# Performance work log

Measured on AMD Instinct MI355X. Metric: run time of the kernel, lower is better.

The kernel has to match this reference:

```python
import jax, jax.numpy as jnp
import numpy as np

WIN_LEN = 400
HOP = 100
NFFT = 512


def _make_kernel():
    # rfft of identity -> DFT basis, truncated to window length
    fb = np.fft.rfft(np.eye(NFFT))[:WIN_LEN]          # [WIN_LEN, NFFT//2+1] complex
    kernel = np.concatenate([fb.real, fb.imag], axis=1).T  # [2*(NFFT//2+1), WIN_LEN]
    # periodic (fftbins=True) Hamming window, as scipy.signal.get_window('hamming', N, fftbins=True)
    n = np.arange(WIN_LEN)
    window = (0.54 - 0.46 * np.cos(2.0 * np.pi * n / WIN_LEN)).astype(np.float32)
    kernel = kernel.astype(np.float32)[:, None, :] * window  # [514, 1, WIN_LEN]
    return jnp.asarray(kernel)


def setup_inputs() -> dict:
    key = jax.random.key(0)
    x = jax.random.normal(key, (32, 480000), dtype=jnp.float32)  # [B, T] raw audio
    return {"x": x, "weight": _make_kernel()}


def reference(x, weight):
    # x: [B, T] -> [B, 1, T]; pad both sides by (window_len - hop)
    pad = WIN_LEN - HOP
    xp = jnp.pad(x[:, None, :], ((0, 0), (0, 0), (pad, pad)))
    # strided conv against fixed Fourier basis -> [B, 2*(NFFT//2+1), n_frames]
    out = jax.lax.conv_general_dilated(
        xp, weight,
        window_strides=(HOP,),
        padding='VALID',
        dimension_numbers=('NCH', 'OIH', 'NCH'),
    )
    return out
```

## Files before the change

kernel.cpp:

```cpp
#include <hip/hip_runtime.h>
#include <hip/hip_bf16.h>


#define T_LEN   480000
#define NF      4803
#define C_OUT   514
#define HOP     100
#define WIN     400
#define BM      128
#define BN      64
#define WSTR    424
#define XPS     487040
#define XP_TOTAL (32 * XPS)
#define WP_ROWS 576
#define WP_ELEMS (WP_ROWS * WSTR)
#define WP_BYTE_OFF ((size_t)XP_TOTAL * 2)
#define WS_NEEDED (WP_BYTE_OFF + (size_t)WP_ELEMS * 2)
#define MT_CNT  38
#define NT_CNT  9
#define NTILES  (NT_CNT * MT_CNT * 32)
#define TPNT    (MT_CNT * 32)
#define XSEG    13312
#define NBLK    512

typedef __attribute__((ext_vector_type(8))) short short8;
typedef __attribute__((ext_vector_type(4))) float f32x4;

__device__ __forceinline__ unsigned short f2bf(float f) {
    unsigned int u = __float_as_uint(f);
    u += 0x7FFFu + ((u >> 16) & 1u);
    return (unsigned short)(u >> 16);
}

__device__ __forceinline__ void gl_lds16(const unsigned short* g, unsigned short* l) {
    __builtin_amdgcn_global_load_lds(
        (const __attribute__((address_space(1))) unsigned int*)(g),
        (__attribute__((address_space(3))) unsigned int*)(l), 16, 0, 0);
}

__global__ void cvt_x_kernel(const float* __restrict__ x, unsigned short* __restrict__ xp) {
    const int t = blockIdx.x * 256 + threadIdx.x;
    const int b  = t / (XPS / 4);
    const int i4 = t - b * (XPS / 4);
    const int i  = i4 * 4;
    const int g  = i - 300;
    ushort4 h;
    if (g >= 0 && g + 3 < T_LEN) {
        const float4 f = *(const float4*)(x + (size_t)b * T_LEN + g);
        h.x = f2bf(f.x); h.y = f2bf(f.y); h.z = f2bf(f.z); h.w = f2bf(f.w);
    } else {
        const float* xb = x + (size_t)b * T_LEN;
        h.x = (g + 0 >= 0 && g + 0 < T_LEN) ? f2bf(xb[g + 0]) : 0;
        h.y = (g + 1 >= 0 && g + 1 < T_LEN) ? f2bf(xb[g + 1]) : 0;
        h.z = (g + 2 >= 0 && g + 2 < T_LEN) ? f2bf(xb[g + 2]) : 0;
        h.w = (g + 3 >= 0 && g + 3 < T_LEN) ? f2bf(xb[g + 3]) : 0;
    }
    *(ushort4*)(xp + (size_t)b * XPS + i) = h;
}

__global__ void cvt_w_kernel(const float* __restrict__ w, unsigned short* __restrict__ wp) {
    const int t = blockIdx.x * 256 + threadIdx.x;
    if (t >= WP_ELEMS) return;
    const int c = t / WSTR;
    const int k = t - c * WSTR;
    wp[t] = (c < C_OUT && k < WIN) ? f2bf(w[(size_t)c * WIN + k]) : 0;
}

__device__ __forceinline__ void decode_tile(int t, int& nt, int& b, int& mt) {
    nt = t / TPNT;
    const int rem = t - nt * TPNT;
    b  = rem / MT_CNT;
    mt = rem - b * MT_CNT;
}

__global__ __launch_bounds__(512, 4)
void stft_gemm(const unsigned short* __restrict__ xp,
               const unsigned short* __restrict__ wp,
               float* __restrict__ out) {
    __shared__ unsigned short w_s[BN * WSTR];
    __shared__ unsigned short x_s[XSEG];

    const int tid  = threadIdx.x;
    const int lane = tid & 63;
    const int wv   = tid >> 6;

    const int id  = blockIdx.x;
    const int t0  = id * 21 + ((id < 192) ? id : 192);
    const int nti = 21 + (id < 192 ? 1 : 0);

    int nt, b, mt;
    decode_tile(t0, nt, b, mt);

    {
        const unsigned short* wg = wp + (size_t)nt * (BN * WSTR);
        #pragma unroll
        for (int c = wv; c < 53; c += 8) {
            const int idx = (c << 6) + lane;
            gl_lds16(wg + idx * 8, w_s + idx * 8);
        }
        const unsigned short* xg = xp + (size_t)b * XPS + mt * (BM * HOP);
        #pragma unroll
        for (int c = wv; c < 26; c += 8) {
            const int idx = (c << 6) + lane;
            gl_lds16(xg + idx * 8, x_s + idx * 8);
        }
    }
    __syncthreads();

    const int q4 = lane >> 4;
    const int lm = lane & 15;
    const int wr = wv & 3;
    const int wc = wv >> 2;

    int aoff[2];
    #pragma unroll
    for (int mi = 0; mi < 2; ++mi) aoff[mi] = (wr * 32 + mi * 16 + lm) * HOP + q4 * 8;
    int boff[2];
    #pragma unroll
    for (int ni = 0; ni < 2; ++ni) boff[ni] = (wc * 32 + ni * 16 + lm) * WSTR + q4 * 8;

    for (int ti = 0; ti < nti; ++ti) {
        f32x4 acc[2][2];
        #pragma unroll
        for (int mi = 0; mi < 2; ++mi)
            #pragma unroll
            for (int ni = 0; ni < 2; ++ni)
                acc[mi][ni] = (f32x4){0.f, 0.f, 0.f, 0.f};

        #pragma unroll
        for (int kc = 0; kc < 13; ++kc) {
            const int k = kc * 32;
            union { short8 v; unsigned long long u[2]; } au[2];
            #pragma unroll
            for (int mi = 0; mi < 2; ++mi) {
                const unsigned long long* p = (const unsigned long long*)(x_s + aoff[mi] + k);
                au[mi].u[0] = p[0]; au[mi].u[1] = p[1];
            }
            #pragma unroll
            for (int ni = 0; ni < 2; ++ni) {
                const short8 bf = *(const short8*)(&w_s[boff[ni] + k]);
                #pragma unroll
                for (int mi = 0; mi < 2; ++mi)
                    acc[mi][ni] = __builtin_amdgcn_mfma_f32_16x16x32_bf16(au[mi].v, bf, acc[mi][ni], 0, 0, 0);
            }
        }

        __syncthreads();

        int nnt = nt, nb = 0, nmt = 0;
        const bool have_next = (ti + 1 < nti);
        if (have_next) {
            decode_tile(t0 + ti + 1, nnt, nb, nmt);
            const unsigned short* xg = xp + (size_t)nb * XPS + nmt * (BM * HOP);
            #pragma unroll
            for (int c = wv; c < 26; c += 8) {
                const int idx = (c << 6) + lane;
                gl_lds16(xg + idx * 8, x_s + idx * 8);
            }
            if (nnt != nt) {
                const unsigned short* wg = wp + (size_t)nnt * (BN * WSTR);
                #pragma unroll
                for (int c = wv; c < 53; c += 8) {
                    const int idx = (c << 6) + lane;
                    gl_lds16(wg + idx * 8, w_s + idx * 8);
                }
            }
        }

        float* ob = out + (size_t)b * C_OUT * NF;
        const int f_base = mt * BM + wr * 32 + q4 * 4;
        const int c_base = nt * BN + wc * 32 + lm;
        #pragma unroll
        for (int mi = 0; mi < 2; ++mi) {
            const int fg = f_base + mi * 16;
            const bool fok = (fg + 3 < NF);
            #pragma unroll
            for (int ni = 0; ni < 2; ++ni) {
                const int cg = c_base + ni * 16;
                if (cg < C_OUT) {
                    float* op = ob + (size_t)cg * NF + fg;
                    if (fok) {
                        op[0] = acc[mi][ni][0]; op[1] = acc[mi][ni][1];
                        op[2] = acc[mi][ni][2]; op[3] = acc[mi][ni][3];
                    } else {
                        #pragma unroll
                        for (int rI = 0; rI < 4; ++rI)
                            if (fg + rI < NF) op[rI] = acc[mi][ni][rI];
                    }
                }
            }
        }

        __syncthreads();
        nt = nnt; b = nb; mt = nmt;
    }
}

#define SEG 13120
__global__ __launch_bounds__(256, 2)
void conv_stft_fallback(const float* __restrict__ x,
                        const float* __restrict__ w,
                        float* __restrict__ out) {
    __shared__ short x_s[SEG];
    __shared__ short w_s[BN * WSTR];
    const int tid = threadIdx.x;
    const int nt  = blockIdx.x;
    const int mt  = blockIdx.y;
    const int b   = blockIdx.z;
    const int s0 = mt * (BM * HOP) - 300;
    const float* xb = x + (size_t)b * T_LEN;
    for (int v = tid; v < SEG / 4; v += 256) {
        int g = s0 + v * 4;
        float f0, f1, f2, f3;
        if (g >= 0 && g + 3 < T_LEN) {
            const float4 f = *(const float4*)(xb + g);
            f0 = f.x; f1 = f.y; f2 = f.z; f3 = f.w;
        } else {
            f0 = (g + 0 >= 0 && g + 0 < T_LEN) ? xb[g + 0] : 0.f;
            f1 = (g + 1 >= 0 && g + 1 < T_LEN) ? xb[g + 1] : 0.f;
            f2 = (g + 2 >= 0 && g + 2 < T_LEN) ? xb[g + 2] : 0.f;
            f3 = (g + 3 >= 0 && g + 3 < T_LEN) ? xb[g + 3] : 0.f;
        }
        ushort4 h; h.x = f2bf(f0); h.y = f2bf(f1); h.z = f2bf(f2); h.w = f2bf(f3);
        *(ushort4*)(&x_s[v * 4]) = h;
    }
    for (int s = tid; s < BN * 106; s += 256) {
        const int r  = s / 106;
        const int gk = s - r * 106;
        const int c  = nt * BN + r;
        ushort4 h = make_ushort4(0, 0, 0, 0);
        if (gk < 100 && c < C_OUT) {
            const float4 f = *(const float4*)(w + (size_t)c * WIN + gk * 4);
            h.x = f2bf(f.x); h.y = f2bf(f.y); h.z = f2bf(f.z); h.w = f2bf(f.w);
        }
        if (gk * 4 < WSTR) *(ushort4*)(&w_s[r * WSTR + gk * 4]) = h;
    }
    __syncthreads();
    const int lane = tid & 63, wv = tid >> 6, q = lane >> 4, lm = lane & 15;
    f32x4 acc[2][4];
    #pragma unroll
    for (int mi = 0; mi < 2; ++mi)
        #pragma unroll
        for (int ni = 0; ni < 4; ++ni) acc[mi][ni] = (f32x4){0.f,0.f,0.f,0.f};
    const int a0 = (wv * 32 + lm) * HOP + q * 8;
    const int a1 = a0 + 16 * HOP;
    int boff[4];
    #pragma unroll
    for (int ni = 0; ni < 4; ++ni) boff[ni] = (ni * 16 + lm) * WSTR + q * 8;
    #pragma unroll
    for (int kc = 0; kc < 13; ++kc) {
        const int k = kc * 32;
        union { short8 v; unsigned long long u[2]; } au0, au1;
        const unsigned long long* p0 = (const unsigned long long*)(x_s + a0 + k);
        const unsigned long long* p1 = (const unsigned long long*)(x_s + a1 + k);
        au0.u[0] = p0[0]; au0.u[1] = p0[1];
        au1.u[0] = p1[0]; au1.u[1] = p1[1];
        #pragma unroll
        for (int ni = 0; ni < 4; ++ni) {
            const short8 bf = *(const short8*)(&w_s[boff[ni] + k]);
            acc[0][ni] = __builtin_amdgcn_mfma_f32_16x16x32_bf16(au0.v, bf, acc[0][ni], 0, 0, 0);
            acc[1][ni] = __builtin_amdgcn_mfma_f32_16x16x32_bf16(au1.v, bf, acc[1][ni], 0, 0, 0);
        }
    }
    float* ob = out + (size_t)b * C_OUT * NF;
    const int f_base = mt * BM + wv * 32 + q * 4;
    const int c_base = nt * BN + lm;
    #pragma unroll
    for (int mi = 0; mi < 2; ++mi) {
        #pragma unroll
        for (int ni = 0; ni < 4; ++ni) {
            const int cg = c_base + ni * 16;
            if (cg < C_OUT) {
                float* op = ob + (size_t)cg * NF;
                #pragma unroll
                for (int r = 0; r < 4; ++r) {
                    const int fg = f_base + mi * 16 + r;
                    if (fg < NF) op[fg] = acc[mi][ni][r];
                }
            }
        }
    }
}

extern "C" void kernel_launch(void* const* d_in, const int* in_sizes, int n_in,
                              void* d_out, int out_size, void* d_ws, size_t ws_size,
                              hipStream_t stream) {
    const float* x = (const float*)d_in[0];
    const float* w = (const float*)d_in[1];
    float* out = (float*)d_out;

    if (ws_size >= WS_NEEDED) {
        unsigned short* xp = (unsigned short*)d_ws;
        unsigned short* wp = (unsigned short*)((char*)d_ws + WP_BYTE_OFF);
        cvt_x_kernel<<<XP_TOTAL / 4 / 256, 256, 0, stream>>>(x, xp);
        cvt_w_kernel<<<(WP_ELEMS + 255) / 256, 256, 0, stream>>>(w, wp);
        stft_gemm<<<dim3(NBLK), 512, 0, stream>>>(xp, wp, out);
    } else {
        dim3 grid(NT_CNT, MT_CNT, 32);
        conv_stft_fallback<<<grid, 256, 0, stream>>>(x, w, out);
    }
}
```

Before: 460.2 us.

## Stream pre-swizzled B fragments from global and loop all N-tiles per x segment

Weights are converted into an MFMA-fragment-ordered bf16 layout so each lane reads its B operand directly from global (L2-resident) memory, and the LDS copy of the weights is removed. Each block now owns whole x segments and loops over all nine N tiles, so each segment is loaded into LDS once instead of once per N tile. This reduces LDS footprint and x reload traffic. In exchange, B operands now come from global memory in the inner loop with no prefetch, and x loads are no longer overlapped with the epilogue.

```diff
diff --git a/kernel.cpp b/kernel.cpp
--- a/kernel.cpp
+++ b/kernel.cpp
@@ -12,16 +12,15 @@
 #define WSTR    424
 #define XPS     487040
 #define XP_TOTAL (32 * XPS)
-#define WP_ROWS 576
-#define WP_ELEMS (WP_ROWS * WSTR)
-#define WP_BYTE_OFF ((size_t)XP_TOTAL * 2)
-#define WS_NEEDED (WP_BYTE_OFF + (size_t)WP_ELEMS * 2)
 #define MT_CNT  38
 #define NT_CNT  9
-#define NTILES  (NT_CNT * MT_CNT * 32)
-#define TPNT    (MT_CNT * 32)
+#define NSEG    (MT_CNT * 32)
 #define XSEG    13312
 #define NBLK    512
+#define WP2_CH    (NT_CNT * 13 * 4 * 64)
+#define WP2_ELEMS (WP2_CH * 8)
+#define WP2_BYTE_OFF ((size_t)XP_TOTAL * 2)
+#define WS_NEEDED (WP2_BYTE_OFF + (size_t)WP2_ELEMS * 2)
 
 typedef __attribute__((ext_vector_type(8))) short short8;
 typedef __attribute__((ext_vector_type(4))) float f32x4;
@@ -58,54 +57,48 @@
     *(ushort4*)(xp + (size_t)b * XPS + i) = h;
 }
 
-__global__ void cvt_w_kernel(const float* __restrict__ w, unsigned short* __restrict__ wp) {
+__global__ void cvt_w2_kernel(const float* __restrict__ w, unsigned short* __restrict__ wp2) {
     const int t = blockIdx.x * 256 + threadIdx.x;
-    if (t >= WP_ELEMS) return;
-    const int c = t / WSTR;
-    const int k = t - c * WSTR;
-    wp[t] = (c < C_OUT && k < WIN) ? f2bf(w[(size_t)c * WIN + k]) : 0;
-}
-
-__device__ __forceinline__ void decode_tile(int t, int& nt, int& b, int& mt) {
-    nt = t / TPNT;
-    const int rem = t - nt * TPNT;
-    b  = rem / MT_CNT;
-    mt = rem - b * MT_CNT;
+    if (t >= WP2_CH) return;
+    const int lane = t & 63;
+    int r = t >> 6;
+    const int cb = r & 3; r >>= 2;
+    const int kc = r % 13;
+    const int nt = r / 13;
+    const int chan = nt * 64 + cb * 16 + (lane & 15);
+    const int k0   = kc * 32 + (lane >> 4) * 8;
+    unsigned short h[8];
+    #pragma unroll
+    for (int j = 0; j < 8; ++j) {
+        const int k = k0 + j;
+        h[j] = (chan < C_OUT && k < WIN) ? f2bf(w[(size_t)chan * WIN + k]) : (unsigned short)0;
+    }
+    uint4 u;
+    u.x = (unsigned)h[0] | ((unsigned)h[1] << 16);
+    u.y = (unsigned)h[2] | ((unsigned)h[3] << 16);
+    u.z = (unsigned)h[4] | ((unsigned)h[5] << 16);
+    u.w = (unsigned)h[6] | ((unsigned)h[7] << 16);
+    *(uint4*)(wp2 + (size_t)t * 8) = u;
+}
+
+__device__ __forceinline__ short8 ldB(const unsigned short* __restrict__ wp2,
+                                      int nt, int kc, int cb, int lane) {
+    return *(const short8*)(wp2 + (size_t)((((nt * 13 + kc) * 4 + cb) << 6) + lane) * 8);
 }
 
 __global__ __launch_bounds__(512, 4)
 void stft_gemm(const unsigned short* __restrict__ xp,
-               const unsigned short* __restrict__ wp,
+               const unsigned short* __restrict__ wp2,
                float* __restrict__ out) {
-    __shared__ unsigned short w_s[BN * WSTR];
     __shared__ unsigned short x_s[XSEG];
 
     const int tid  = threadIdx.x;
     const int lane = tid & 63;
     const int wv   = tid >> 6;
 
-    const int id  = blockIdx.x;
-    const int t0  = id * 21 + ((id < 192) ? id : 192);
-    const int nti = 21 + (id < 192 ? 1 : 0);
-
-    int nt, b, mt;
-    decode_tile(t0, nt, b, mt);
-
-    {
-        const unsigned short* wg = wp + (size_t)nt * (BN * WSTR);
-        #pragma unroll
-        for (int c = wv; c < 53; c += 8) {
-            const int idx = (c << 6) + lane;
-            gl_lds16(wg + idx * 8, w_s + idx * 8);
-        }
-        const unsigned short* xg = xp + (size_t)b * XPS + mt * (BM * HOP);
-        #pragma unroll
-        for (int c = wv; c < 26; c += 8) {
-            const int idx = (c << 6) + lane;
-            gl_lds16(xg + idx * 8, x_s + idx * 8);
-        }
-    }
-    __syncthreads();
+    const int id   = blockIdx.x;
+    const int s0   = (id < 192) ? id * 3 : 576 + (id - 192) * 2;
+    const int nseg = (id < 192) ? 3 : 2;
 
     const int q4 = lane >> 4;
     const int lm = lane & 15;
@@ -115,84 +108,73 @@
     int aoff[2];
     #pragma unroll
     for (int mi = 0; mi < 2; ++mi) aoff[mi] = (wr * 32 + mi * 16 + lm) * HOP + q4 * 8;
-    int boff[2];
-    #pragma unroll
-    for (int ni = 0; ni < 2; ++ni) boff[ni] = (wc * 32 + ni * 16 + lm) * WSTR + q4 * 8;
-
-    for (int ti = 0; ti < nti; ++ti) {
-        f32x4 acc[2][2];
-        #pragma unroll
-        for (int mi = 0; mi < 2; ++mi)
-            #pragma unroll
-            for (int ni = 0; ni < 2; ++ni)
-                acc[mi][ni] = (f32x4){0.f, 0.f, 0.f, 0.f};
-
-        #pragma unroll
-        for (int kc = 0; kc < 13; ++kc) {
-            const int k = kc * 32;
-            union { short8 v; unsigned long long u[2]; } au[2];
-            #pragma unroll
-            for (int mi = 0; mi < 2; ++mi) {
-                const unsigned long long* p = (const unsigned long long*)(x_s + aoff[mi] + k);
-                au[mi].u[0] = p[0]; au[mi].u[1] = p[1];
-            }
-            #pragma unroll
-            for (int ni = 0; ni < 2; ++ni) {
-                const short8 bf = *(const short8*)(&w_s[boff[ni] + k]);
-                #pragma unroll
-                for (int mi = 0; mi < 2; ++mi)
-                    acc[mi][ni] = __builtin_amdgcn_mfma_f32_16x16x32_bf16(au[mi].v, bf, acc[mi][ni], 0, 0, 0);
-            }
-        }
+
+    for (int si = 0; si < nseg; ++si) {
+        const int s  = s0 + si;
+        const int b  = s / MT_CNT;
+        const int mt = s - b * MT_CNT;
 
         __syncthreads();
-
-        int nnt = nt, nb = 0, nmt = 0;
-        const bool have_next = (ti + 1 < nti);
-        if (have_next) {
-            decode_tile(t0 + ti + 1, nnt, nb, nmt);
-            const unsigned short* xg = xp + (size_t)nb * XPS + nmt * (BM * HOP);
+        {
+            const unsigned short* xg = xp + (size_t)b * XPS + mt * (BM * HOP);
             #pragma unroll
             for (int c = wv; c < 26; c += 8) {
                 const int idx = (c << 6) + lane;
                 gl_lds16(xg + idx * 8, x_s + idx * 8);
             }
-            if (nnt != nt) {
-                const unsigned short* wg = wp + (size_t)nnt * (BN * WSTR);
-                #pragma unroll
-                for (int c = wv; c < 53; c += 8) {
-                    const int idx = (c << 6) + lane;
-                    gl_lds16(wg + idx * 8, w_s + idx * 8);
-                }
-            }
-        }
-
-        float* ob = out + (size_t)b * C_OUT * NF;
-        const int f_base = mt * BM + wr * 32 + q4 * 4;
-        const int c_base = nt * BN + wc * 32 + lm;
-        #pragma unroll
-        for (int mi = 0; mi < 2; ++mi) {
-            const int fg = f_base + mi * 16;
-            const bool fok = (fg + 3 < NF);
-            #pragma unroll
-            for (int ni = 0; ni < 2; ++ni) {
-                const int cg = c_base + ni * 16;
-                if (cg < C_OUT) {
-                    float* op = ob + (size_t)cg * NF + fg;
-                    if (fok) {
-                        op[0] = acc[mi][ni][0]; op[1] = acc[mi][ni][1];
-                        op[2] = acc[mi][ni][2]; op[3] = acc[mi][ni][3];
-                    } else {
-                        #pragma unroll
-                        for (int rI = 0; rI < 4; ++rI)
-                            if (fg + rI < NF) op[rI] = acc[mi][ni][rI];
+        }
+        __syncthreads();
+
+        for (int nt = 0; nt < NT_CNT; ++nt) {
+            f32x4 acc[2][2];
+            #pragma unroll
+            for (int mi = 0; mi < 2; ++mi)
+                #pragma unroll
+                for (int ni = 0; ni < 2; ++ni)
+                    acc[mi][ni] = (f32x4){0.f, 0.f, 0.f, 0.f};
+
+            #pragma unroll
+            for (int kc = 0; kc < 13; ++kc) {
+                const int k = kc * 32;
+                union { short8 v; unsigned long long u[2]; } au[2];
+                #pragma unroll
+                for (int mi = 0; mi < 2; ++mi) {
+                    const unsigned long long* p = (const unsigned long long*)(x_s + aoff[mi] + k);
+                    au[mi].u[0] = p[0]; au[mi].u[1] = p[1];
+                }
+                const short8 b0 = ldB(wp2, nt, kc, wc * 2 + 0, lane);
+                const short8 b1 = ldB(wp2, nt, kc, wc * 2 + 1, lane);
+                #pragma unroll
+                for (int mi = 0; mi < 2; ++mi) {
+                    acc[mi][0] = __builtin_amdgcn_mfma_f32_16x16x32_bf16(au[mi].v, b0, acc[mi][0], 0, 0, 0);
+                    acc[mi][1] = __builtin_amdgcn_mfma_f32_16x16x32_bf16(au[mi].v, b1, acc[mi][1], 0, 0, 0);
+                }
+            }
+
+            float* ob = out + (size_t)b * C_OUT * NF;
+            const int f_base = mt * BM + wr * 32 + q4 * 4;
+            const int c_base = nt * BN + wc * 32 + lm;
+            #pragma unroll
+            for (int mi = 0; mi < 2; ++mi) {
+                const int fg = f_base + mi * 16;
+                const bool fok = (fg + 3 < NF);
+                #pragma unroll
+                for (int ni = 0; ni < 2; ++ni) {
+                    const int cg = c_base + ni * 16;
+                    if (cg < C_OUT) {
+                        float* op = ob + (size_t)cg * NF + fg;
+                        if (fok) {
+                            op[0] = acc[mi][ni][0]; op[1] = acc[mi][ni][1];
+                            op[2] = acc[mi][ni][2]; op[3] = acc[mi][ni][3];
+                        } else {
+                            #pragma unroll
+                            for (int rI = 0; rI < 4; ++rI)
+                                if (fg + rI < NF) op[rI] = acc[mi][ni][rI];
+                        }
                     }
                 }
             }
         }
-
-        __syncthreads();
-        nt = nnt; b = nb; mt = nmt;
     }
 }
 
@@ -290,11 +272,11 @@
     float* out = (float*)d_out;
 
     if (ws_size >= WS_NEEDED) {
-        unsigned short* xp = (unsigned short*)d_ws;
-        unsigned short* wp = (unsigned short*)((char*)d_ws + WP_BYTE_OFF);
+        unsigned short* xp  = (unsigned short*)d_ws;
+        unsigned short* wp2 = (unsigned short*)((char*)d_ws + WP2_BYTE_OFF);
         cvt_x_kernel<<<XP_TOTAL / 4 / 256, 256, 0, stream>>>(x, xp);
-        cvt_w_kernel<<<(WP_ELEMS + 255) / 256, 256, 0, stream>>>(w, wp);
-        stft_gemm<<<dim3(NBLK), 512, 0, stream>>>(xp, wp, out);
+        cvt_w2_kernel<<<(WP2_CH + 255) / 256, 256, 0, stream>>>(w, wp2);
+        stft_gemm<<<dim3(NBLK), 512, 0, stream>>>(xp, wp2, out);
     } else {
         dim3 grid(NT_CNT, MT_CNT, 32);
         conv_stft_fallback<<<grid, 256, 0, stream>>>(x, w, out);
```

Measured after the change: 697.9 us. +51.7%, slower.
